# Kernel tuning notes

Measured on AMD Instinct MI355X. Metric: run time of the kernel, lower is better.

## Reference

```python
import jax, jax.numpy as jnp
import numpy as np

# decoded layout constants
NN, NO, SD = 16, 8, 4          # num_neighbors, num_obstacles, state_dim_per_agent
B = 131072                      # batch rows
H1, E, HP, AD = 64, 16, 64, 2   # phi hidden, embed, psi hidden, action dim
D_ROBOT, D_OBST = 0.3, 0.3
B_GAMMA, B_EXPH = 0.05, 1.0
PHI_MIN, PHI_MAX = -2.0, 2.0
A_MAX = 2.0


def setup_inputs() -> dict:
    key = jax.random.key(0)
    kx, kw = jax.random.split(key)
    # x: [count | goal(SD) | NN neighbor rel-states (SD each) | NO obstacle rel-pos (2 each)]
    x = jax.random.normal(kx, (B, 1 + SD + SD * NN + 2 * NO), dtype=jnp.float32) * 2.0
    x = x.at[:, 0].set(float(NN))
    names = [("Wp1n", (SD, H1)), ("bp1n", (H1,)), ("Wp2n", (H1, E)), ("bp2n", (E,)),
             ("Wr1n", (E, H1)), ("br1n", (H1,)), ("Wr2n", (H1, E)), ("br2n", (E,)),
             ("Wp1o", (2, H1)), ("bp1o", (H1,)), ("Wp2o", (H1, E)), ("bp2o", (E,)),
             ("Wr1o", (E, H1)), ("br1o", (H1,)), ("Wr2o", (H1, E)), ("br2o", (E,)),
             ("Wpsi1", (2 * E + SD, HP)), ("bpsi1", (HP,)), ("Wpsi2", (HP, AD)), ("bpsi2", (AD,))]
    ks = jax.random.split(kw, len(names))
    inp = {"x": x}
    for (n, sh), k in zip(names, ks):
        s = 1.0 / np.sqrt(sh[0])  # torch Linear default init scale
        inp[n] = jax.random.uniform(k, sh, jnp.float32, -s, s)
    return inp


def _mlp2(h, W1, b1, W2, b2):
    # Feedforward: activation between layers, linear output
    return jax.nn.relu(h @ W1 + b1) @ W2 + b2


def _deepset(el, Wp1, bp1, Wp2, bp2, Wr1, br1, Wr2, br2):
    # el: [B, n, d] -> phi each element, sum over set, rho
    phi = _mlp2(el, Wp1, bp1, Wp2, bp2)          # [B, n, E]
    return _mlp2(phi.sum(axis=1), Wr1, br1, Wr2, br2)  # [B, E]


def _barrier_sum(P, D):
    # P: [B, n, 2]; APF barrier gamma * P / (|P| * (|P|-D)^exph), summed over n
    nrm = jnp.linalg.norm(P, axis=-1, keepdims=True)   # [B, n, 1]
    H = nrm - D
    return (B_GAMMA * P / (nrm * H ** B_EXPH)).sum(axis=1)  # [B, 2]


def reference(x, Wp1n, bp1n, Wp2n, bp2n, Wr1n, br1n, Wr2n, br2n,
              Wp1o, bp1o, Wp2o, bp2o, Wr1o, br1o, Wr2o, br2o,
              Wpsi1, bpsi1, Wpsi2, bpsi2):
    nb = x.shape[0]
    g = x[:, 1:1 + SD]                                        # goal
    nbr = x[:, 1 + SD:1 + SD + SD * NN].reshape(nb, NN, SD)   # neighbor rel-states
    obs = x[:, 1 + SD + SD * NN:].reshape(nb, NO, 2)          # obstacle rel-pos

    rho_n = _deepset(nbr, Wp1n, bp1n, Wp2n, bp2n, Wr1n, br1n, Wr2n, br2n)
    rho_o = _deepset(obs, Wp1o, bp1o, Wp2o, bp2o, Wr1o, br1o, Wr2o, br2o)

    h = jnp.concatenate([rho_n, rho_o, g], axis=1)            # [B, 2E+SD]
    emp = _mlp2(h, Wpsi1, bpsi1, Wpsi2, bpsi2)                # psi network
    emp = (jnp.tanh(emp) + 1.0) / 2.0 * (PHI_MAX - PHI_MIN) + PHI_MIN  # scale_empty

    bar = _barrier_sum(-nbr[:, :, :2], D_ROBOT) + _barrier_sum(-obs, D_OBST)

    action = emp + bar
    # scale(): divide rows whose inf-norm exceeds a_max
    inv_alpha = jnp.maximum(jnp.max(jnp.abs(action), axis=1, keepdims=True) / A_MAX, 1.0)
    return action / inv_alpha
```

## Files before the change

kernel.cpp:

```cpp
#include <hip/hip_runtime.h>
#include <math.h>


typedef __attribute__((ext_vector_type(8))) _Float16 f16x8;
typedef __attribute__((ext_vector_type(2))) __fp16 fp16x2;
typedef __attribute__((ext_vector_type(4))) float f32x4;

#define XW 85

#define FR_S1N  0
#define FR_S1O  4
#define FR_G2N  8
#define FR_G2O  10
#define FR_RNA  12
#define FR_RNB  16
#define FR_ROA  18
#define FR_ROB  22
#define FR_PSI1 24
#define FR_PSI2 32
#define N_FRAGS 34

#define BIG_STR 144
#define PHI_STR 80
#define CAT_STR 144
#define L_BIGN 0
#define L_BIGO 2304
#define L_PHN  4608
#define L_PHO  5888
#define L_CAT  7168
#define L_OUT  9472
#define L_BAR  9600
#define L_NBA  9728
#define NBA_STR 136
#define L_OBA  11904
#define OBA_STR 68
#define GRP_LDS 12448

__device__ __forceinline__ float fast_rcp(float x)  { return __builtin_amdgcn_rcpf(x); }
__device__ __forceinline__ float fast_sqrt(float x) { return __builtin_amdgcn_sqrtf(x); }

__device__ __forceinline__ float two_tanh(float a) {
    float ax = fabsf(a);
    float e = __expf(2.0f * ax);
    float t = 1.0f - 2.0f * fast_rcp(e + 1.0f);
    return copysignf(2.0f * t, a);
}

__device__ __forceinline__ void lds_order() {
    __asm__ __volatile__("" ::: "memory");
}

__device__ __forceinline__ unsigned pk2(float a, float b) {
    union { fp16x2 h; unsigned u; } t;
    t.h = __builtin_amdgcn_cvt_pkrtz(a, b);
    return t.u;
}
__device__ __forceinline__ f16x8 lds_af(const char* area, int stride, int off, int lane) {
    int mm = lane & 15, qq = lane >> 4;
    return *(const f16x8*)(area + mm * stride + off + qq * 16);
}
__device__ __forceinline__ f16x8 load_bh(const _Float16* wsf, int frag, int lane) {
    return ((const f16x8*)(wsf + (size_t)frag * 512))[lane];
}
__device__ __forceinline__ f32x4 cinit(float b) {
    f32x4 c; c[0] = b; c[1] = b; c[2] = b; c[3] = b; return c;
}
__device__ __forceinline__ f32x4 mfma1(f16x8 a, f16x8 b, f32x4 c) {
    return __builtin_amdgcn_mfma_f32_16x16x32_f16(a, b, c, 0, 0, 0);
}

__global__ void bn_prep(const float* __restrict__ Wp1n, const float* __restrict__ Wp2n,
                        const float* __restrict__ Wr1n, const float* __restrict__ Wr2n,
                        const float* __restrict__ Wp1o, const float* __restrict__ Wp2o,
                        const float* __restrict__ Wr1o, const float* __restrict__ Wr2o,
                        const float* __restrict__ Wpsi1, const float* __restrict__ Wpsi2,
                        _Float16* __restrict__ wsf)
{
    int f = blockIdx.x;
    int lane = threadIdx.x;
    const float* W; int K, N, kk = 0, nt = 0, rel;
    if (f < 4)        { W = Wp1n;  K = 4;  N = 64; nt = f; }
    else if (f < 8)   { W = Wp1o;  K = 2;  N = 64; nt = f - 4; }
    else if (f < 10)  { W = Wp2n;  K = 64; N = 16; kk = f - 8; }
    else if (f < 12)  { W = Wp2o;  K = 64; N = 16; kk = f - 10; }
    else if (f < 16)  { W = Wr1n;  K = 16; N = 64; nt = f - 12; }
    else if (f < 18)  { W = Wr2n;  K = 64; N = 16; kk = f - 16; }
    else if (f < 22)  { W = Wr1o;  K = 16; N = 64; nt = f - 18; }
    else if (f < 24)  { W = Wr2o;  K = 64; N = 16; kk = f - 22; }
    else if (f < 32)  { rel = f - 24; W = Wpsi1; K = 36; N = 64; kk = rel >> 2; nt = rel & 3; }
    else              { W = Wpsi2; K = 64; N = 2;  kk = f - 32; }

    int q = lane >> 4, c = lane & 15;
    _Float16* dst = wsf + (size_t)f * 512 + lane * 8;
    for (int j = 0; j < 8; ++j) {
        int k = kk * 32 + q * 8 + j;
        int n = nt * 16 + c;
        float v = (k < K && n < N) ? W[k * N + n] : 0.f;
        dst[j] = (_Float16)v;
    }
}

__global__ __launch_bounds__(256, 4) void bn_main(
    const float* __restrict__ x, const _Float16* __restrict__ wsf,
    const float* __restrict__ bp1n, const float* __restrict__ bp2n,
    const float* __restrict__ br1n, const float* __restrict__ br2n,
    const float* __restrict__ bp1o, const float* __restrict__ bp2o,
    const float* __restrict__ br1o, const float* __restrict__ br2o,
    const float* __restrict__ bpsi1, const float* __restrict__ bpsi2,
    float* __restrict__ out, int nb)
{
    __shared__ char smem[2 * GRP_LDS];
    const int lane = threadIdx.x & 63;
    const int wid  = threadIdx.x >> 6;
    const int grp  = wid >> 1;
    const int role = wid & 1;
    const int group = blockIdx.x * 2 + grp;
    const int row0 = group * 16;

    char* Gl   = smem + grp * GRP_LDS;
    char* BIGN = Gl + L_BIGN;
    char* BIGO = Gl + L_BIGO;
    char* PHN  = Gl + L_PHN;
    char* PHO  = Gl + L_PHO;
    char* CAT  = Gl + L_CAT;
    char* OUTA = Gl + L_OUT;
    char* BAR  = Gl + L_BAR;
    char* NBA  = Gl + L_NBA;
    char* OBA  = Gl + L_OBA;

    const int m = lane & 15, q = lane >> 4, c = m;
    const float* xg   = x + (size_t)row0 * XW;
    const float* xrow = xg + (size_t)m * XW;

    if (role == 0) {
        {
            int ln5 = lane >> 5;
            int pr  = lane & 31;
            int mm0 = pr >> 1, fp = pr & 1;
            char* db = NBA + mm0 * NBA_STR + fp * 4;
            const float* s0 = xg + (size_t)ln5 * XW + 5 + pr * 2;
            #pragma unroll
            for (int t = 0; t < 8; ++t) {
                const float* s = s0 + (size_t)(2 * t) * XW;
                *(unsigned*)(db + (2 * t + ln5) * 8) = pk2(s[0], s[1]);
            }
        }

        for (int i = lane; i < 128; i += 64) {
            int r = i >> 3, d = i & 7;
            *(unsigned*)(PHN + r * PHI_STR + 32 + d * 4) = 0;
        }
        lds_order();

        float b_s1n[4], b_rna[4];
        #pragma unroll
        for (int nt = 0; nt < 4; ++nt) {
            b_s1n[nt] = bp1n[nt * 16 + c];
            b_rna[nt] = br1n[nt * 16 + c];
        }
        float b_g2n = 16.f * bp2n[c];
        float b_rnb = br2n[c];

        f16x8 Bs1n[4], Bg2n[2];
        #pragma unroll
        for (int nt = 0; nt < 4; ++nt) Bs1n[nt] = load_bh(wsf, FR_S1N + nt, lane);
        Bg2n[0] = load_bh(wsf, FR_G2N + 0, lane);
        Bg2n[1] = load_bh(wsf, FR_G2N + 1, lane);

        {
            const int m8 = m * 8;
            f32x4 acc[4];
            #pragma unroll
            for (int nt = 0; nt < 4; ++nt) acc[nt] = cinit(0.f);
            #pragma unroll 8
            for (int mm = 0; mm < 16; ++mm) {
                union { f16x8 v; unsigned u[4]; uint2 h[2]; } A;
                A.h[0] = *(const uint2*)(NBA + mm * NBA_STR + m8);
                A.u[2] = 0; A.u[3] = 0;
                #pragma unroll
                for (int nt = 0; nt < 4; ++nt) {
                    f32x4 cc = mfma1(A.v, Bs1n[nt], cinit(b_s1n[nt]));
                    #pragma unroll
                    for (int reg = 0; reg < 4; ++reg)
                        acc[nt][reg] += fmaxf(cc[reg], 0.f);
                }
            }
            #pragma unroll
            for (int nt = 0; nt < 4; ++nt)
                #pragma unroll
                for (int reg = 0; reg < 4; ++reg)
                    *(_Float16*)(BIGN + (q * 4 + reg) * BIG_STR + (nt * 16 + c) * 2)
                        = (_Float16)acc[nt][reg];
        }
        f16x8 Brna[4];
        #pragma unroll
        for (int nt = 0; nt < 4; ++nt) Brna[nt] = load_bh(wsf, FR_RNA + nt, lane);
        lds_order();

        {
            f16x8 A0 = lds_af(BIGN, BIG_STR, 0, lane);
            f16x8 A1 = lds_af(BIGN, BIG_STR, 64, lane);
            f32x4 ca = mfma1(A0, Bg2n[0], cinit(b_g2n));
            f32x4 cb = mfma1(A1, Bg2n[1], cinit(0.f));
            #pragma unroll
            for (int reg = 0; reg < 4; ++reg)
                *(_Float16*)(PHN + (q * 4 + reg) * PHI_STR + c * 2) = (_Float16)(ca[reg] + cb[reg]);
        }
        f16x8 Brnb[2];
        Brnb[0] = load_bh(wsf, FR_RNB + 0, lane);
        Brnb[1] = load_bh(wsf, FR_RNB + 1, lane);
        lds_order();

        {
            f16x8 A = lds_af(PHN, PHI_STR, 0, lane);
            #pragma unroll
            for (int nt = 0; nt < 4; ++nt) {
                f32x4 cc = mfma1(A, Brna[nt], cinit(b_rna[nt]));
                #pragma unroll
                for (int reg = 0; reg < 4; ++reg)
                    *(_Float16*)(BIGN + (q * 4 + reg) * BIG_STR + (nt * 16 + c) * 2) = (_Float16)fmaxf(cc[reg], 0.f);
            }
        }
        lds_order();

        {
            f16x8 A0 = lds_af(BIGN, BIG_STR, 0, lane);
            f16x8 A1 = lds_af(BIGN, BIG_STR, 64, lane);
            f32x4 ca = mfma1(A0, Brnb[0], cinit(b_rnb));
            f32x4 cb = mfma1(A1, Brnb[1], cinit(0.f));
            #pragma unroll
            for (int reg = 0; reg < 4; ++reg)
                *(_Float16*)(CAT + (q * 4 + reg) * CAT_STR + c * 2) = (_Float16)(ca[reg] + cb[reg]);
        }
    } else {
        {
            int r8 = lane >> 3;
            int oo = lane & 7;
            char* db = OBA + oo * OBA_STR;
            const float* s0 = xg + (size_t)r8 * XW + 69 + oo * 2;
            #pragma unroll
            for (int t = 0; t < 2; ++t) {
                const float* s = s0 + (size_t)(8 * t) * XW;
                *(unsigned*)(db + (8 * t + r8) * 4) = pk2(s[0], s[1]);
            }
        }

        for (int i = lane; i < 128; i += 64) {
            int r = i >> 3, d = i & 7;
            *(unsigned*)(PHO + r * PHI_STR + 32 + d * 4) = 0;
        }
        for (int i = lane; i < 256; i += 64) {
            int r = i >> 4, d = i & 15;
            *(unsigned*)(CAT + r * CAT_STR + 64 + d * 4) = 0;
        }
        lds_order();

        if (lane < 16) {
            const float* xr = x + (size_t)(row0 + lane) * XW;
            uint2 gv;
            gv.x = pk2(xr[1], xr[2]);
            gv.y = pk2(xr[3], xr[4]);
            *(uint2*)(CAT + lane * CAT_STR + 64) = gv;
        }

        {
            float bx = 0.f, by = 0.f;
            #pragma unroll
            for (int i = 0; i < 4; ++i) {
                int n = 4 * q + i;
                float px = -xrow[5 + 4 * n], py = -xrow[6 + 4 * n];
                float nrm = fast_sqrt(px * px + py * py);
                float coef = 0.05f * fast_rcp(nrm * (nrm - 0.3f));
                bx = fmaf(coef, px, bx);
                by = fmaf(coef, py, by);
            }
            #pragma unroll
            for (int i = 0; i < 2; ++i) {
                int o = 2 * q + i;
                float px = -xrow[69 + 2 * o], py = -xrow[70 + 2 * o];
                float nrm = fast_sqrt(px * px + py * py);
                float coef = 0.05f * fast_rcp(nrm * (nrm - 0.3f));
                bx = fmaf(coef, px, bx);
                by = fmaf(coef, py, by);
            }
            bx += __shfl_xor(bx, 16); by += __shfl_xor(by, 16);
            bx += __shfl_xor(bx, 32); by += __shfl_xor(by, 32);
            if (q == 0) { float2 bb; bb.x = bx; bb.y = by; *(float2*)(BAR + m * 8) = bb; }
        }

        float b_s1o[4], b_roa[4];
        #pragma unroll
        for (int nt = 0; nt < 4; ++nt) {
            b_s1o[nt] = bp1o[nt * 16 + c];
            b_roa[nt] = br1o[nt * 16 + c];
        }
        float b_g2o = 8.f * bp2o[c];
        float b_rob = br2o[c];

        f16x8 Bs1o[4], Bg2o[2];
        #pragma unroll
        for (int nt = 0; nt < 4; ++nt) Bs1o[nt] = load_bh(wsf, FR_S1O + nt, lane);
        Bg2o[0] = load_bh(wsf, FR_G2O + 0, lane);
        Bg2o[1] = load_bh(wsf, FR_G2O + 1, lane);

        {
            const int m4 = m * 4;
            f32x4 acc[4];
            #pragma unroll
            for (int nt = 0; nt < 4; ++nt) acc[nt] = cinit(0.f);
            #pragma unroll
            for (int oo = 0; oo < 8; ++oo) {
                union { f16x8 v; unsigned u[4]; } A;
                A.u[0] = *(const unsigned*)(OBA + oo * OBA_STR + m4);
                A.u[1] = 0; A.u[2] = 0; A.u[3] = 0;
                #pragma unroll
                for (int nt = 0; nt < 4; ++nt) {
                    f32x4 cc = mfma1(A.v, Bs1o[nt], cinit(b_s1o[nt]));
                    #pragma unroll
                    for (int reg = 0; reg < 4; ++reg)
                        acc[nt][reg] += fmaxf(cc[reg], 0.f);
                }
            }
            #pragma unroll
            for (int nt = 0; nt < 4; ++nt)
                #pragma unroll
                for (int reg = 0; reg < 4; ++reg)
                    *(_Float16*)(BIGO + (q * 4 + reg) * BIG_STR + (nt * 16 + c) * 2)
                        = (_Float16)acc[nt][reg];
        }
        f16x8 Broa[4];
        #pragma unroll
        for (int nt = 0; nt < 4; ++nt) Broa[nt] = load_bh(wsf, FR_ROA + nt, lane);
        lds_order();

        {
            f16x8 A0 = lds_af(BIGO, BIG_STR, 0, lane);
            f16x8 A1 = lds_af(BIGO, BIG_STR, 64, lane);
            f32x4 ca = mfma1(A0, Bg2o[0], cinit(b_g2o));
            f32x4 cb = mfma1(A1, Bg2o[1], cinit(0.f));
            #pragma unroll
            for (int reg = 0; reg < 4; ++reg)
                *(_Float16*)(PHO + (q * 4 + reg) * PHI_STR + c * 2) = (_Float16)(ca[reg] + cb[reg]);
        }
        f16x8 Brob[2];
        Brob[0] = load_bh(wsf, FR_ROB + 0, lane);
        Brob[1] = load_bh(wsf, FR_ROB + 1, lane);
        lds_order();

        {
            f16x8 A = lds_af(PHO, PHI_STR, 0, lane);
            #pragma unroll
            for (int nt = 0; nt < 4; ++nt) {
                f32x4 cc = mfma1(A, Broa[nt], cinit(b_roa[nt]));
                #pragma unroll
                for (int reg = 0; reg < 4; ++reg)
                    *(_Float16*)(BIGO + (q * 4 + reg) * BIG_STR + (nt * 16 + c) * 2) = (_Float16)fmaxf(cc[reg], 0.f);
            }
        }
        lds_order();

        {
            f16x8 A0 = lds_af(BIGO, BIG_STR, 0, lane);
            f16x8 A1 = lds_af(BIGO, BIG_STR, 64, lane);
            f32x4 ca = mfma1(A0, Brob[0], cinit(b_rob));
            f32x4 cb = mfma1(A1, Brob[1], cinit(0.f));
            #pragma unroll
            for (int reg = 0; reg < 4; ++reg)
                *(_Float16*)(CAT + (q * 4 + reg) * CAT_STR + (16 + c) * 2) = (_Float16)(ca[reg] + cb[reg]);
        }
    }

    __syncthreads();

    if (role == 1) {
        float b_p1[4];
        #pragma unroll
        for (int nt = 0; nt < 4; ++nt) b_p1[nt] = bpsi1[nt * 16 + c];
        float b_p2 = (c < 2) ? bpsi2[c] : 0.f;

        f16x8 Bp1a[4], Bp1b[4], Bp2[2];
        #pragma unroll
        for (int nt = 0; nt < 4; ++nt) Bp1a[nt] = load_bh(wsf, FR_PSI1 + nt, lane);
        #pragma unroll
        for (int nt = 0; nt < 4; ++nt) Bp1b[nt] = load_bh(wsf, FR_PSI1 + 4 + nt, lane);
        Bp2[0] = load_bh(wsf, FR_PSI2 + 0, lane);
        Bp2[1] = load_bh(wsf, FR_PSI2 + 1, lane);

        {
            f16x8 A0 = lds_af(CAT, CAT_STR, 0, lane);
            f16x8 A1 = lds_af(CAT, CAT_STR, 64, lane);
            #pragma unroll
            for (int nt = 0; nt < 4; ++nt) {
                f32x4 ca = mfma1(A0, Bp1a[nt], cinit(b_p1[nt]));
                f32x4 cb = mfma1(A1, Bp1b[nt], cinit(0.f));
                #pragma unroll
                for (int reg = 0; reg < 4; ++reg)
                    *(_Float16*)(BIGO + (q * 4 + reg) * BIG_STR + (nt * 16 + c) * 2) = (_Float16)fmaxf(ca[reg] + cb[reg], 0.f);
            }
        }
        lds_order();

        {
            f16x8 A0 = lds_af(BIGO, BIG_STR, 0, lane);
            f16x8 A1 = lds_af(BIGO, BIG_STR, 64, lane);
            f32x4 ca = mfma1(A0, Bp2[0], cinit(b_p2));
            f32x4 cb = mfma1(A1, Bp2[1], cinit(0.f));
            if (c < 2) {
                #pragma unroll
                for (int reg = 0; reg < 4; ++reg)
                    *(float*)(OUTA + (q * 4 + reg) * 8 + c * 4) = ca[reg] + cb[reg];
            }
        }
        lds_order();

        if (lane < 16) {
            float2 a  = *(const float2*)(OUTA + lane * 8);
            float2 bb = *(const float2*)(BAR + lane * 8);
            float a0 = two_tanh(a.x) + bb.x;
            float a1 = two_tanh(a.y) + bb.y;
            float amax = fmaxf(fabsf(a0), fabsf(a1));
            float inv_alpha = fmaxf(amax * 0.5f, 1.0f);
            float rr = fast_rcp(inv_alpha);
            float2 o; o.x = a0 * rr; o.y = a1 * rr;
            *(float2*)(out + (size_t)(row0 + lane) * 2) = o;
        }
    }
}

extern "C" void kernel_launch(void* const* d_in, const int* in_sizes, int n_in,
                              void* d_out, int out_size, void* d_ws, size_t ws_size,
                              hipStream_t stream) {
    const float* x     = (const float*)d_in[0];
    const float* Wp1n  = (const float*)d_in[1];
    const float* bp1n  = (const float*)d_in[2];
    const float* Wp2n  = (const float*)d_in[3];
    const float* bp2n  = (const float*)d_in[4];
    const float* Wr1n  = (const float*)d_in[5];
    const float* br1n  = (const float*)d_in[6];
    const float* Wr2n  = (const float*)d_in[7];
    const float* br2n  = (const float*)d_in[8];
    const float* Wp1o  = (const float*)d_in[9];
    const float* bp1o  = (const float*)d_in[10];
    const float* Wp2o  = (const float*)d_in[11];
    const float* bp2o  = (const float*)d_in[12];
    const float* Wr1o  = (const float*)d_in[13];
    const float* br1o  = (const float*)d_in[14];
    const float* Wr2o  = (const float*)d_in[15];
    const float* br2o  = (const float*)d_in[16];
    const float* Wpsi1 = (const float*)d_in[17];
    const float* bpsi1 = (const float*)d_in[18];
    const float* Wpsi2 = (const float*)d_in[19];
    const float* bpsi2 = (const float*)d_in[20];
    float* out = (float*)d_out;

    int nb = in_sizes[0] / XW;
    _Float16* wsf = (_Float16*)d_ws;

    bn_prep<<<N_FRAGS, 64, 0, stream>>>(Wp1n, Wp2n, Wr1n, Wr2n,
                                        Wp1o, Wp2o, Wr1o, Wr2o,
                                        Wpsi1, Wpsi2, wsf);

    int groups = (nb + 15) / 16;
    int blocks = (groups + 1) / 2;
    bn_main<<<blocks, 256, 0, stream>>>(x, wsf,
                                        bp1n, bp2n, br1n, br2n,
                                        bp1o, bp2o, br1o, br2o,
                                        bpsi1, bpsi2, out, nb);
}
```

Baseline: 146.1 us.

## Fold layer-1 biases into MFMA weights, alias staging LDS, raise occupancy

First-layer biases move into the packed fp16 weight fragments as an extra K row, and the A operands get a constant 1.0 in the matching slot, so per-lane bias registers and their loads go away. The neighbor and obstacle staging buffers now alias the BIG scratch areas, which shrinks LDS per group and needs extra ordering barriers. Weight fragment loads are deferred to just before use, and launch bounds rise to 8 blocks per SIMD. The aim is lower register and LDS pressure so more waves stay resident, at the cost of rounding the biases to fp16 and possible load latency exposed by the late loads.

```diff
diff --git a/kernel.cpp b/kernel.cpp
--- a/kernel.cpp
+++ b/kernel.cpp
@@ -30,11 +30,11 @@
 #define L_CAT  7168
 #define L_OUT  9472
 #define L_BAR  9600
-#define L_NBA  9728
+#define GRP_LDS 9728
 #define NBA_STR 136
-#define L_OBA  11904
 #define OBA_STR 68
-#define GRP_LDS 12448
+
+#define H16_ONE 0x00003C00u
 
 __device__ __forceinline__ float fast_rcp(float x)  { return __builtin_amdgcn_rcpf(x); }
 __device__ __forceinline__ float fast_sqrt(float x) { return __builtin_amdgcn_sqrtf(x); }
@@ -74,20 +74,25 @@
                         const float* __restrict__ Wp1o, const float* __restrict__ Wp2o,
                         const float* __restrict__ Wr1o, const float* __restrict__ Wr2o,
                         const float* __restrict__ Wpsi1, const float* __restrict__ Wpsi2,
+                        const float* __restrict__ bp1n, const float* __restrict__ bp1o,
+                        const float* __restrict__ br1n, const float* __restrict__ br1o,
+                        const float* __restrict__ bpsi1,
                         _Float16* __restrict__ wsf)
 {
     int f = blockIdx.x;
     int lane = threadIdx.x;
-    const float* W; int K, N, kk = 0, nt = 0, rel;
-    if (f < 4)        { W = Wp1n;  K = 4;  N = 64; nt = f; }
-    else if (f < 8)   { W = Wp1o;  K = 2;  N = 64; nt = f - 4; }
+    const float* W; const float* bias = nullptr;
+    int K, N, kk = 0, nt = 0, rel, kbias = -1;
+    if (f < 4)        { W = Wp1n;  K = 4;  N = 64; nt = f;      bias = bp1n;  kbias = 4; }
+    else if (f < 8)   { W = Wp1o;  K = 2;  N = 64; nt = f - 4;  bias = bp1o;  kbias = 2; }
     else if (f < 10)  { W = Wp2n;  K = 64; N = 16; kk = f - 8; }
     else if (f < 12)  { W = Wp2o;  K = 64; N = 16; kk = f - 10; }
-    else if (f < 16)  { W = Wr1n;  K = 16; N = 64; nt = f - 12; }
+    else if (f < 16)  { W = Wr1n;  K = 16; N = 64; nt = f - 12; bias = br1n;  kbias = 16; }
     else if (f < 18)  { W = Wr2n;  K = 64; N = 16; kk = f - 16; }
-    else if (f < 22)  { W = Wr1o;  K = 16; N = 64; nt = f - 18; }
+    else if (f < 22)  { W = Wr1o;  K = 16; N = 64; nt = f - 18; bias = br1o;  kbias = 16; }
     else if (f < 24)  { W = Wr2o;  K = 64; N = 16; kk = f - 22; }
-    else if (f < 32)  { rel = f - 24; W = Wpsi1; K = 36; N = 64; kk = rel >> 2; nt = rel & 3; }
+    else if (f < 32)  { rel = f - 24; W = Wpsi1; K = 36; N = 64; kk = rel >> 2; nt = rel & 3;
+                        bias = bpsi1; kbias = 36; }
     else              { W = Wpsi2; K = 64; N = 2;  kk = f - 32; }
 
     int q = lane >> 4, c = lane & 15;
@@ -95,18 +100,20 @@
     for (int j = 0; j < 8; ++j) {
         int k = kk * 32 + q * 8 + j;
         int n = nt * 16 + c;
-        float v = (k < K && n < N) ? W[k * N + n] : 0.f;
+        float v = 0.f;
+        if (n < N) {
+            if (k < K) v = W[k * N + n];
+            else if (k == kbias) v = bias[n];
+        }
         dst[j] = (_Float16)v;
     }
 }
 
-__global__ __launch_bounds__(256, 4) void bn_main(
+__global__ __launch_bounds__(256, 8) void bn_main(
     const float* __restrict__ x, const _Float16* __restrict__ wsf,
-    const float* __restrict__ bp1n, const float* __restrict__ bp2n,
-    const float* __restrict__ br1n, const float* __restrict__ br2n,
-    const float* __restrict__ bp1o, const float* __restrict__ bp2o,
-    const float* __restrict__ br1o, const float* __restrict__ br2o,
-    const float* __restrict__ bpsi1, const float* __restrict__ bpsi2,
+    const float* __restrict__ bp2n, const float* __restrict__ br2n,
+    const float* __restrict__ bp2o, const float* __restrict__ br2o,
+    const float* __restrict__ bpsi2,
     float* __restrict__ out, int nb)
 {
     __shared__ char smem[2 * GRP_LDS];
@@ -125,12 +132,14 @@
     char* CAT  = Gl + L_CAT;
     char* OUTA = Gl + L_OUT;
     char* BAR  = Gl + L_BAR;
-    char* NBA  = Gl + L_NBA;
-    char* OBA  = Gl + L_OBA;
+    char* NBA  = BIGN;
+    char* OBA  = BIGO;
 
     const int m = lane & 15, q = lane >> 4, c = m;
     const float* xg   = x + (size_t)row0 * XW;
     const float* xrow = xg + (size_t)m * XW;
+
+    const f32x4 ZC = cinit(0.f);
 
     if (role == 0) {
         {
@@ -146,45 +155,38 @@
             }
         }
 
-        for (int i = lane; i < 128; i += 64) {
-            int r = i >> 3, d = i & 7;
-            *(unsigned*)(PHN + r * PHI_STR + 32 + d * 4) = 0;
-        }
-        lds_order();
-
-        float b_s1n[4], b_rna[4];
-        #pragma unroll
-        for (int nt = 0; nt < 4; ++nt) {
-            b_s1n[nt] = bp1n[nt * 16 + c];
-            b_rna[nt] = br1n[nt * 16 + c];
-        }
-        float b_g2n = 16.f * bp2n[c];
-        float b_rnb = br2n[c];
-
-        f16x8 Bs1n[4], Bg2n[2];
+        {
+            unsigned zv = ((lane & 7) == 0) ? H16_ONE : 0u;
+            for (int i = lane; i < 128; i += 64) {
+                int r = i >> 3, d = i & 7;
+                *(unsigned*)(PHN + r * PHI_STR + 32 + d * 4) = zv;
+            }
+        }
+        lds_order();
+
+        f16x8 Bs1n[4];
         #pragma unroll
         for (int nt = 0; nt < 4; ++nt) Bs1n[nt] = load_bh(wsf, FR_S1N + nt, lane);
-        Bg2n[0] = load_bh(wsf, FR_G2N + 0, lane);
-        Bg2n[1] = load_bh(wsf, FR_G2N + 1, lane);
 
         {
             const int m8 = m * 8;
             f32x4 acc[4];
             #pragma unroll
             for (int nt = 0; nt < 4; ++nt) acc[nt] = cinit(0.f);
+            union { f16x8 v; unsigned u[4]; uint2 h[2]; } A;
+            A.u[2] = H16_ONE; A.u[3] = 0;
             #pragma unroll 8
             for (int mm = 0; mm < 16; ++mm) {
-                union { f16x8 v; unsigned u[4]; uint2 h[2]; } A;
                 A.h[0] = *(const uint2*)(NBA + mm * NBA_STR + m8);
-                A.u[2] = 0; A.u[3] = 0;
                 #pragma unroll
                 for (int nt = 0; nt < 4; ++nt) {
-                    f32x4 cc = mfma1(A.v, Bs1n[nt], cinit(b_s1n[nt]));
+                    f32x4 cc = mfma1(A.v, Bs1n[nt], ZC);
                     #pragma unroll
                     for (int reg = 0; reg < 4; ++reg)
                         acc[nt][reg] += fmaxf(cc[reg], 0.f);
                 }
             }
+            lds_order();
             #pragma unroll
             for (int nt = 0; nt < 4; ++nt)
                 #pragma unroll
@@ -192,30 +194,30 @@
                     *(_Float16*)(BIGN + (q * 4 + reg) * BIG_STR + (nt * 16 + c) * 2)
                         = (_Float16)acc[nt][reg];
         }
-        f16x8 Brna[4];
-        #pragma unroll
-        for (int nt = 0; nt < 4; ++nt) Brna[nt] = load_bh(wsf, FR_RNA + nt, lane);
-        lds_order();
-
-        {
+        lds_order();
+
+        {
+            float b_g2n = 16.f * bp2n[c];
+            f16x8 Bg2n0 = load_bh(wsf, FR_G2N + 0, lane);
+            f16x8 Bg2n1 = load_bh(wsf, FR_G2N + 1, lane);
             f16x8 A0 = lds_af(BIGN, BIG_STR, 0, lane);
             f16x8 A1 = lds_af(BIGN, BIG_STR, 64, lane);
-            f32x4 ca = mfma1(A0, Bg2n[0], cinit(b_g2n));
-            f32x4 cb = mfma1(A1, Bg2n[1], cinit(0.f));
+            f32x4 ca = mfma1(A0, Bg2n0, cinit(b_g2n));
+            f32x4 cb = mfma1(A1, Bg2n1, ZC);
             #pragma unroll
             for (int reg = 0; reg < 4; ++reg)
                 *(_Float16*)(PHN + (q * 4 + reg) * PHI_STR + c * 2) = (_Float16)(ca[reg] + cb[reg]);
         }
-        f16x8 Brnb[2];
-        Brnb[0] = load_bh(wsf, FR_RNB + 0, lane);
-        Brnb[1] = load_bh(wsf, FR_RNB + 1, lane);
-        lds_order();
-
-        {
+        lds_order();
+
+        {
+            f16x8 Brna[4];
+            #pragma unroll
+            for (int nt = 0; nt < 4; ++nt) Brna[nt] = load_bh(wsf, FR_RNA + nt, lane);
             f16x8 A = lds_af(PHN, PHI_STR, 0, lane);
             #pragma unroll
             for (int nt = 0; nt < 4; ++nt) {
-                f32x4 cc = mfma1(A, Brna[nt], cinit(b_rna[nt]));
+                f32x4 cc = mfma1(A, Brna[nt], ZC);
                 #pragma unroll
                 for (int reg = 0; reg < 4; ++reg)
                     *(_Float16*)(BIGN + (q * 4 + reg) * BIG_STR + (nt * 16 + c) * 2) = (_Float16)fmaxf(cc[reg], 0.f);
@@ -224,10 +226,13 @@
         lds_order();
 
         {
+            float b_rnb = br2n[c];
+            f16x8 Brnb0 = load_bh(wsf, FR_RNB + 0, lane);
+            f16x8 Brnb1 = load_bh(wsf, FR_RNB + 1, lane);
             f16x8 A0 = lds_af(BIGN, BIG_STR, 0, lane);
             f16x8 A1 = lds_af(BIGN, BIG_STR, 64, lane);
-            f32x4 ca = mfma1(A0, Brnb[0], cinit(b_rnb));
-            f32x4 cb = mfma1(A1, Brnb[1], cinit(0.f));
+            f32x4 ca = mfma1(A0, Brnb0, cinit(b_rnb));
+            f32x4 cb = mfma1(A1, Brnb1, ZC);
             #pragma unroll
             for (int reg = 0; reg < 4; ++reg)
                 *(_Float16*)(CAT + (q * 4 + reg) * CAT_STR + c * 2) = (_Float16)(ca[reg] + cb[reg]);
@@ -245,13 +250,19 @@
             }
         }
 
-        for (int i = lane; i < 128; i += 64) {
-            int r = i >> 3, d = i & 7;
-            *(unsigned*)(PHO + r * PHI_STR + 32 + d * 4) = 0;
-        }
-        for (int i = lane; i < 256; i += 64) {
-            int r = i >> 4, d = i & 15;
-            *(unsigned*)(CAT + r * CAT_STR + 64 + d * 4) = 0;
+        {
+            unsigned zv = ((lane & 7) == 0) ? H16_ONE : 0u;
+            for (int i = lane; i < 128; i += 64) {
+                int r = i >> 3, d = i & 7;
+                *(unsigned*)(PHO + r * PHI_STR + 32 + d * 4) = zv;
+            }
+        }
+        {
+            unsigned zc = ((lane & 15) == 2) ? H16_ONE : 0u;
+            for (int i = lane; i < 256; i += 64) {
+                int r = i >> 4, d = i & 15;
+                *(unsigned*)(CAT + r * CAT_STR + 64 + d * 4) = zc;
+            }
         }
         lds_order();
 
@@ -288,39 +299,29 @@
             if (q == 0) { float2 bb; bb.x = bx; bb.y = by; *(float2*)(BAR + m * 8) = bb; }
         }
 
-        float b_s1o[4], b_roa[4];
-        #pragma unroll
-        for (int nt = 0; nt < 4; ++nt) {
-            b_s1o[nt] = bp1o[nt * 16 + c];
-            b_roa[nt] = br1o[nt * 16 + c];
-        }
-        float b_g2o = 8.f * bp2o[c];
-        float b_rob = br2o[c];
-
-        f16x8 Bs1o[4], Bg2o[2];
+        f16x8 Bs1o[4];
         #pragma unroll
         for (int nt = 0; nt < 4; ++nt) Bs1o[nt] = load_bh(wsf, FR_S1O + nt, lane);
-        Bg2o[0] = load_bh(wsf, FR_G2O + 0, lane);
-        Bg2o[1] = load_bh(wsf, FR_G2O + 1, lane);
 
         {
             const int m4 = m * 4;
             f32x4 acc[4];
             #pragma unroll
             for (int nt = 0; nt < 4; ++nt) acc[nt] = cinit(0.f);
+            union { f16x8 v; unsigned u[4]; } A;
+            A.u[1] = H16_ONE; A.u[2] = 0; A.u[3] = 0;
             #pragma unroll
             for (int oo = 0; oo < 8; ++oo) {
-                union { f16x8 v; unsigned u[4]; } A;
                 A.u[0] = *(const unsigned*)(OBA + oo * OBA_STR + m4);
-                A.u[1] = 0; A.u[2] = 0; A.u[3] = 0;
                 #pragma unroll
                 for (int nt = 0; nt < 4; ++nt) {
-                    f32x4 cc = mfma1(A.v, Bs1o[nt], cinit(b_s1o[nt]));
+                    f32x4 cc = mfma1(A.v, Bs1o[nt], ZC);
                     #pragma unroll
                     for (int reg = 0; reg < 4; ++reg)
                         acc[nt][reg] += fmaxf(cc[reg], 0.f);
                 }
             }
+            lds_order();
             #pragma unroll
             for (int nt = 0; nt < 4; ++nt)
                 #pragma unroll
@@ -328,30 +329,30 @@
                     *(_Float16*)(BIGO + (q * 4 + reg) * BIG_STR + (nt * 16 + c) * 2)
                         = (_Float16)acc[nt][reg];
         }
-        f16x8 Broa[4];
-        #pragma unroll
-        for (int nt = 0; nt < 4; ++nt) Broa[nt] = load_bh(wsf, FR_ROA + nt, lane);
-        lds_order();
-
-        {
+        lds_order();
+
+        {
+            float b_g2o = 8.f * bp2o[c];
+            f16x8 Bg2o0 = load_bh(wsf, FR_G2O + 0, lane);
+            f16x8 Bg2o1 = load_bh(wsf, FR_G2O + 1, lane);
             f16x8 A0 = lds_af(BIGO, BIG_STR, 0, lane);
             f16x8 A1 = lds_af(BIGO, BIG_STR, 64, lane);
-            f32x4 ca = mfma1(A0, Bg2o[0], cinit(b_g2o));
-            f32x4 cb = mfma1(A1, Bg2o[1], cinit(0.f));
+            f32x4 ca = mfma1(A0, Bg2o0, cinit(b_g2o));
+            f32x4 cb = mfma1(A1, Bg2o1, ZC);
             #pragma unroll
             for (int reg = 0; reg < 4; ++reg)
                 *(_Float16*)(PHO + (q * 4 + reg) * PHI_STR + c * 2) = (_Float16)(ca[reg] + cb[reg]);
         }
-        f16x8 Brob[2];
-        Brob[0] = load_bh(wsf, FR_ROB + 0, lane);
-        Brob[1] = load_bh(wsf, FR_ROB + 1, lane);
-        lds_order();
-
-        {
+        lds_order();
+
+        {
+            f16x8 Broa[4];
+            #pragma unroll
+            for (int nt = 0; nt < 4; ++nt) Broa[nt] = load_bh(wsf, FR_ROA + nt, lane);
             f16x8 A = lds_af(PHO, PHI_STR, 0, lane);
             #pragma unroll
             for (int nt = 0; nt < 4; ++nt) {
-                f32x4 cc = mfma1(A, Broa[nt], cinit(b_roa[nt]));
+                f32x4 cc = mfma1(A, Broa[nt], ZC);
                 #pragma unroll
                 for (int reg = 0; reg < 4; ++reg)
                     *(_Float16*)(BIGO + (q * 4 + reg) * BIG_STR + (nt * 16 + c) * 2) = (_Float16)fmaxf(cc[reg], 0.f);
@@ -360,10 +361,13 @@
         lds_order();
 
         {
+            float b_rob = br2o[c];
+            f16x8 Brob0 = load_bh(wsf, FR_ROB + 0, lane);
+            f16x8 Brob1 = load_bh(wsf, FR_ROB + 1, lane);
             f16x8 A0 = lds_af(BIGO, BIG_STR, 0, lane);
             f16x8 A1 = lds_af(BIGO, BIG_STR, 64, lane);
-            f32x4 ca = mfma1(A0, Brob[0], cinit(b_rob));
-            f32x4 cb = mfma1(A1, Brob[1], cinit(0.f));
+            f32x4 ca = mfma1(A0, Brob0, cinit(b_rob));
+            f32x4 cb = mfma1(A1, Brob1, ZC);
             #pragma unroll
             for (int reg = 0; reg < 4; ++reg)
                 *(_Float16*)(CAT + (q * 4 + reg) * CAT_STR + (16 + c) * 2) = (_Float16)(ca[reg] + cb[reg]);
@@ -373,11 +377,6 @@
     __syncthreads();
 
     if (role == 1) {
-        float b_p1[4];
-        #pragma unroll
-        for (int nt = 0; nt < 4; ++nt) b_p1[nt] = bpsi1[nt * 16 + c];
-        float b_p2 = (c < 2) ? bpsi2[c] : 0.f;
-
         f16x8 Bp1a[4], Bp1b[4], Bp2[2];
         #pragma unroll
         for (int nt = 0; nt < 4; ++nt) Bp1a[nt] = load_bh(wsf, FR_PSI1 + nt, lane);
@@ -391,8 +390,8 @@
             f16x8 A1 = lds_af(CAT, CAT_STR, 64, lane);
             #pragma unroll
             for (int nt = 0; nt < 4; ++nt) {
-                f32x4 ca = mfma1(A0, Bp1a[nt], cinit(b_p1[nt]));
-                f32x4 cb = mfma1(A1, Bp1b[nt], cinit(0.f));
+                f32x4 ca = mfma1(A0, Bp1a[nt], ZC);
+                f32x4 cb = mfma1(A1, Bp1b[nt], ZC);
                 #pragma unroll
                 for (int reg = 0; reg < 4; ++reg)
                     *(_Float16*)(BIGO + (q * 4 + reg) * BIG_STR + (nt * 16 + c) * 2) = (_Float16)fmaxf(ca[reg] + cb[reg], 0.f);
@@ -401,10 +400,11 @@
         lds_order();
 
         {
+            float b_p2 = (c < 2) ? bpsi2[c] : 0.f;
             f16x8 A0 = lds_af(BIGO, BIG_STR, 0, lane);
             f16x8 A1 = lds_af(BIGO, BIG_STR, 64, lane);
             f32x4 ca = mfma1(A0, Bp2[0], cinit(b_p2));
-            f32x4 cb = mfma1(A1, Bp2[1], cinit(0.f));
+            f32x4 cb = mfma1(A1, Bp2[1], ZC);
             if (c < 2) {
                 #pragma unroll
                 for (int reg = 0; reg < 4; ++reg)
@@ -458,12 +458,13 @@
 
     bn_prep<<<N_FRAGS, 64, 0, stream>>>(Wp1n, Wp2n, Wr1n, Wr2n,
                                         Wp1o, Wp2o, Wr1o, Wr2o,
-                                        Wpsi1, Wpsi2, wsf);
+                                        Wpsi1, Wpsi2,
+                                        bp1n, bp1o, br1n, br1o, bpsi1,
+                                        wsf);
 
     int groups = (nb + 15) / 16;
     int blocks = (groups + 1) / 2;
     bn_main<<<blocks, 256, 0, stream>>>(x, wsf,
-                                        bp1n, bp2n, br1n, br2n,
-                                        bp1o, bp2o, br1o, br2o,
-                                        bpsi1, bpsi2, out, nb);
-}
+                                        bp2n, br2n, bp2o, br2o, bpsi2,
+                                        out, nb);
+}
```

After: 145.4 us. Within noise of the previous version (-0.5%).
